# Performance work log

Measured on AMD Instinct MI355X. Metric: run time of the kernel, lower is better.

## Reference

```python
import jax, jax.numpy as jnp
import numpy as np

EPS = 1e-8  # F.cosine_similarity eps


def _cosine(nb, q):
    # nb: [N1, k, d], q: [N1, d] -> [N1, k]
    dot = jnp.einsum('nkd,nd->nk', nb, q)
    nb_norm = jnp.maximum(jnp.linalg.norm(nb, axis=-1), EPS)
    q_norm = jnp.maximum(jnp.linalg.norm(q, axis=-1), EPS)[:, None]
    return dot / (nb_norm * q_norm)


def setup_inputs() -> dict:
    key = jax.random.key(0)
    k0, k1, k2, k3 = jax.random.split(key, 4)
    N1, N2, D = 2048, 50000, 512
    return {
        'query_emb0': jax.random.normal(k0, (N1, D), dtype=jnp.float32),
        'query_emb1': jax.random.normal(k1, (N1, D), dtype=jnp.float32),
        'cand_emb0': jax.random.normal(k2, (N2, D), dtype=jnp.float32),
        'cand_emb1': jax.random.normal(k3, (N2, D), dtype=jnp.float32),
        'k': 32,
    }


def reference(query_emb0, query_emb1, cand_emb0, cand_emb1, k):
    # --- get_KNN_batch: L2 cdist on the ORIGINAL embeddings only (matches torch) ---
    # ||q - c||^2 = ||q||^2 + ||c||^2 - 2 q.c  (GEMM-based, compute-bound)
    q2 = jnp.sum(query_emb0 * query_emb0, axis=1, keepdims=True)       # [N1,1]
    c2 = jnp.sum(cand_emb0 * cand_emb0, axis=1)[None, :]               # [1,N2]
    d2 = jnp.maximum(q2 + c2 - 2.0 * (query_emb0 @ cand_emb0.T), 0.0)  # [N1,N2]
    dist = jnp.sqrt(d2)
    # topk of -distance == k nearest
    _, top_k_idx = jax.lax.top_k(-dist, k)                             # [N1,k]

    # --- get_neighbor_embeddings: gather both tables ---
    nb0 = cand_emb0[top_k_idx]  # [N1,k,d]
    nb1 = cand_emb1[top_k_idx]  # [N1,k,d]

    # --- compute_cosine_batch: elementwise max of the two cosine tables ---
    cos0 = _cosine(nb0, query_emb0)
    cos1 = _cosine(nb1, query_emb1)
    cosine_table = jnp.where(cos0 > cos1, cos0, cos1)                  # [N1,k]
    return cosine_table, jnp.mean(cosine_table, axis=-1)
```

## Files before the change

### kernel.cpp

```cpp
#include <hip/hip_runtime.h>
#include <math.h>


#define D       512
#define KSEL    32
#define NSELMX  64
#define NCF     8
#define TOPL    5
#define CEPS    1e-8f
#define INF     __builtin_inff()

#define MTF     64
#define NTF     256
#define KCF     32
#define NTHF    512

#define MT      64
#define NT      512
#define KC      64
#define NTH     512

using s16x8  = __attribute__((ext_vector_type(8)))  short;
using f32x16 = __attribute__((ext_vector_type(16))) float;

__device__ __forceinline__ void async16(const void* g, void* s) {
  __builtin_amdgcn_global_load_lds(
      (const __attribute__((address_space(1))) unsigned int*)g,
      (__attribute__((address_space(3))) unsigned int*)s, 16, 0, 0);
}

#define BARL() do { asm volatile("s_waitcnt lgkmcnt(0)" ::: "memory"); \
                    __builtin_amdgcn_s_barrier();                      \
                    asm volatile("" ::: "memory"); } while (0)

__device__ __forceinline__ unsigned int bfhi2(float x0, float x1) {
  unsigned int u0 = __float_as_uint(x0), u1 = __float_as_uint(x1);
  u0 = (u0 + 0x7fffu + ((u0 >> 16) & 1u)) >> 16;
  u1 = (u1 + 0x7fffu + ((u1 >> 16) & 1u)) & 0xffff0000u;
  return u0 | u1;
}

__global__ __launch_bounds__(256) void sumsq_cvt_kernel(
    const float* __restrict__ C, const float* __restrict__ Q,
    float* __restrict__ c2, float* __restrict__ q2,
    unsigned short* __restrict__ Cb, unsigned short* __restrict__ Qb,
    int n2, int n1)
{
  int wid  = threadIdx.x >> 6;
  int lane = threadIdx.x & 63;
  int row  = blockIdx.x * 4 + wid;
  const float* src; float* dst; unsigned short* bdst;
  if (row < n2) { src = C + (size_t)row * D; dst = c2 + row; bdst = Cb + (size_t)row * D; }
  else {
    int r = row - n2; if (r >= n1) return;
    src = Q + (size_t)r * D; dst = q2 + r; bdst = Qb + (size_t)r * D;
  }
  const float4* s4 = (const float4*)src;
  float4 a = s4[2*lane], b = s4[2*lane + 1];
  float s = a.x*a.x + a.y*a.y + a.z*a.z + a.w*a.w
          + b.x*b.x + b.y*b.y + b.z*b.z + b.w*b.w;
  int4 h;
  h.x = (int)bfhi2(a.x, a.y); h.y = (int)bfhi2(a.z, a.w);
  h.z = (int)bfhi2(b.x, b.y); h.w = (int)bfhi2(b.z, b.w);
  *(int4*)(bdst + 8*lane) = h;
  #pragma unroll
  for (int o = 32; o > 0; o >>= 1) s += __shfl_down(s, o, 64);
  if (lane == 0) *dst = s;
}

__global__ __launch_bounds__(256) void rows_sumsq_kernel(
    const float* __restrict__ C, const float* __restrict__ Q,
    float* __restrict__ c2, float* __restrict__ q2, int n2, int n1)
{
  int wid  = threadIdx.x >> 6;
  int lane = threadIdx.x & 63;
  int row  = blockIdx.x * 4 + wid;
  const float* src; float* dst;
  if (row < n2) { src = C + (size_t)row * D; dst = c2 + row; }
  else { int r = row - n2; if (r >= n1) return; src = Q + (size_t)r * D; dst = q2 + r; }
  const float4* s4 = (const float4*)src;
  float4 a = s4[lane], b = s4[lane + 64];
  float s = a.x*a.x + a.y*a.y + a.z*a.z + a.w*a.w
          + b.x*b.x + b.y*b.y + b.z*b.z + b.w*b.w;
  #pragma unroll
  for (int o = 32; o > 0; o >>= 1) s += __shfl_down(s, o, 64);
  if (lane == 0) *dst = s;
}

__device__ inline void worst_reduce(float dIn, int iIn, float& wd, int& wi) {
  float dd = dIn; int ii = iIn;
  #pragma unroll
  for (int o = 1; o <= 16; o <<= 1) {
    float dp = __shfl_xor(dd, o, 64);
    int   ip = __shfl_xor(ii, o, 64);
    bool take = (dp > dd) || (dp == dd && ip > ii);
    dd = take ? dp : dd; ii = take ? ip : ii;
  }
  wd = __shfl(dd, 0, 64); wi = __shfl(ii, 0, 64);
}

__device__ inline void cvt8(const float4 a, const float4 b, int4& hi, int4& lo) {
  float x[8] = {a.x, a.y, a.z, a.w, b.x, b.y, b.z, b.w};
  unsigned int hw[8], lw[8];
  #pragma unroll
  for (int j = 0; j < 8; ++j) {
    unsigned int ux = __float_as_uint(x[j]);
    unsigned int rh = (ux + 0x7fffu + ((ux >> 16) & 1u)) & 0xffff0000u;
    float rl = x[j] - __uint_as_float(rh);
    unsigned int ul = __float_as_uint(rl);
    hw[j] = rh >> 16;
    lw[j] = (ul + 0x7fffu + ((ul >> 16) & 1u)) >> 16;
  }
  hi = make_int4((int)(hw[0]|(hw[1]<<16)), (int)(hw[2]|(hw[3]<<16)),
                 (int)(hw[4]|(hw[5]<<16)), (int)(hw[6]|(hw[7]<<16)));
  lo = make_int4((int)(lw[0]|(lw[1]<<16)), (int)(lw[2]|(lw[3]<<16)),
                 (int)(lw[4]|(lw[5]<<16)), (int)(lw[6]|(lw[7]<<16)));
}

__global__ __launch_bounds__(NTHF, 2) void knn_phase1_bf_kernel(
    const unsigned short* __restrict__ Qb, const unsigned short* __restrict__ Cb,
    const float* __restrict__ q2g, const float* __restrict__ c2g,
    float* __restrict__ tkd, int* __restrict__ tki,
    int n1, int n2, int chunk, int nc)
{
  extern __shared__ char smem[];
  unsigned short* qs = (unsigned short*)smem;
  char* ringb = smem + 65536;
  float* dl   = (float*)(smem + 131072);

  const int tid  = threadIdx.x;
  const int w    = tid >> 6;
  const int l    = tid & 63;
  const int l31  = l & 31;
  const int half = l >> 5;
  const int bid     = blockIdx.x;
  const int chunkid = bid & (NCF - 1);
  const int mbase   = (bid >> 3) * MTF;
  const int cbase0  = chunkid * chunk;
  const int cend    = min(cbase0 + chunk, n2);

  float q2w[8];
  #pragma unroll
  for (int g = 0; g < 8; ++g)
    q2w[g] = q2g[min(mbase + (g>>2)*32 + w*4 + (g&3), n1 - 1)];

  unsigned long long vv[8][TOPL];
  #pragma unroll
  for (int g = 0; g < 8; ++g)
    #pragma unroll
    for (int t = 0; t < TOPL; ++t) vv[g][t] = 0xffffffffffffffffULL;

  float4 c2cur = *(const float4*)(c2g + cbase0 + 4*l);
  float4 c2nxt = c2cur;

  #pragma unroll
  for (int g = 0; g < 8; ++g) {
    int rho = w*8 + g;
    int gq  = min(mbase + rho, n1 - 1);
    const unsigned short* src = Qb + (size_t)gq * D + (size_t)((l ^ (rho & 7)) * 8);
    unsigned short* dst = qs + rho * 512;
    async16(src, dst);
  }

  auto STAGE = [&](int slot, int s4) {
    int t4 = s4 >> 4, kb4 = s4 & 15;
    #pragma unroll
    for (int i = 0; i < 2; ++i) {
      int cl  = w*32 + i*16 + (l >> 2);
      int gr  = cbase0 + t4*NTF + cl;
      int usr = (l & 3) ^ ((cl >> 1) & 3);
      const unsigned short* src = Cb + (size_t)gr * D + kb4*KCF + usr*8;
      unsigned short* dst = (unsigned short*)(ringb + slot*16384) + (w*32 + i*16)*32;
      async16(src, dst);
    }
  };

  f32x16 zf;
  #pragma unroll
  for (int e = 0; e < 16; ++e) zf[e] = 0.f;

  const int nst   = (cend - cbase0 + NTF - 1) / NTF;
  const int total = nst * 16;
  STAGE(0,0); STAGE(1,1); STAGE(2,2); STAGE(3,3);
  asm volatile("s_waitcnt vmcnt(6)" ::: "memory");
  __builtin_amdgcn_s_barrier();

  f32x16 acc[2];
  acc[0] = zf; acc[1] = zf;

  for (int nt = 0; nt < nst; ++nt) {
    const int cbase = cbase0 + nt * NTF;

    #pragma unroll
    for (int kb = 0; kb < 16; ++kb) {
      const int s   = nt*16 + kb;
      const int rem = total - 1 - s;
      if (rem > 2)       asm volatile("s_waitcnt vmcnt(6)" ::: "memory");
      else if (rem == 2) asm volatile("s_waitcnt vmcnt(4)" ::: "memory");
      else if (rem == 1) asm volatile("s_waitcnt vmcnt(2)" ::: "memory");
      else               asm volatile("s_waitcnt vmcnt(0)" ::: "memory");

      if (kb == 0 && nt + 1 < nst)
        c2nxt = *(const float4*)(c2g + cbase + NTF + 4*l);

      const unsigned short* cb_ =
          (const unsigned short*)(ringb + (s & 3)*16384) + (w*32 + l31)*32;
      #pragma unroll
      for (int ks = 0; ks < 2; ++ks) {
        int uc = (ks*2 + half) ^ ((l31 >> 1) & 3);
        s16x8 cf = *(const s16x8*)(cb_ + uc*8);
        #pragma unroll
        for (int qg = 0; qg < 2; ++qg) {
          int uq = (kb*4 + ks*2 + half) ^ (l31 & 7);
          s16x8 qf = *(const s16x8*)(qs + (qg*32 + l31)*512 + uq*8);
          acc[qg] = __builtin_amdgcn_mfma_f32_32x32x16_bf16(qf, cf, acc[qg], 0, 0, 0);
        }
      }
      if (s + 4 < total) {
        asm volatile("s_waitcnt lgkmcnt(0)" ::: "memory");
        STAGE(s & 3, s + 4);
      }
    }

    #pragma unroll
    for (int p = 0; p < 2; ++p) {
      #pragma unroll
      for (int r = 0; r < 16; ++r) {
        int rr = (r & 3) + 8*(r >> 2) + 4*half;
        dl[rr*NTF + w*32 + l31] = acc[p][r];
      }
      BARL();
      {
        float c2s[4] = {c2cur.x, c2cur.y, c2cur.z, c2cur.w};
        #pragma unroll
        for (int j = 0; j < 4; ++j) {
          const int g = p*4 + j;
          const float q2u = q2w[g];
          float4 sv4 = *((const float4*)(dl + (w*4 + j)*NTF) + l);
          float svs[4] = {sv4.x, sv4.y, sv4.z, sv4.w};
          #pragma unroll
          for (int jj = 0; jj < 4; ++jj) {
            int ci = cbase + 4*l + jj;
            if (ci < cend) {
              float d2v = fmaxf(q2u + c2s[jj] - 2.f*svs[jj], 0.f);
              unsigned long long e =
                  ((unsigned long long)__float_as_uint(d2v) << 32) | (unsigned int)ci;
              if (e < vv[g][TOPL-1]) {
                vv[g][TOPL-1] = e;
                #pragma unroll
                for (int t = TOPL-1; t > 0; --t) {
                  unsigned long long lo = vv[g][t-1] < vv[g][t] ? vv[g][t-1] : vv[g][t];
                  unsigned long long hi = vv[g][t-1] < vv[g][t] ? vv[g][t]   : vv[g][t-1];
                  vv[g][t-1] = lo; vv[g][t] = hi;
                }
              }
            }
          }
        }
      }
      BARL();
      acc[p] = zf;
    }
    c2cur = c2nxt;
  }

  unsigned long long* sel = (unsigned long long*)smem + (size_t)w * 512;
  const unsigned long long mlt = (l == 0) ? 0ull : ((~0ull) >> (64 - l));
  __syncthreads();
  #pragma unroll
  for (int g = 0; g < 8; ++g) {
    unsigned int pk = (unsigned int)(vv[g][0] >> 32);
    #pragma unroll
    for (int o = 1; o < 64; o <<= 1) {
      unsigned int other = (unsigned int)__shfl_xor((int)pk, o, 64);
      pk = (other > pk) ? other : pk;
    }
    int cnt = 0;
    #pragma unroll
    for (int t = 0; t < TOPL; ++t) cnt += ((unsigned int)(vv[g][t] >> 32) <= pk) ? 1 : 0;
    unsigned long long b0 = __ballot(cnt & 1);
    unsigned long long b1 = __ballot(cnt & 2);
    unsigned long long b2 = __ballot(cnt & 4);
    int pre = __popcll(b0 & mlt) + 2*__popcll(b1 & mlt) + 4*__popcll(b2 & mlt);
    int Ns  = __popcll(b0) + 2*__popcll(b1) + 4*__popcll(b2);
    #pragma unroll
    for (int t = 0; t < TOPL; ++t)
      if (t < cnt) sel[pre + t] = vv[g][t];
    asm volatile("s_waitcnt lgkmcnt(0)" ::: "memory");
    __builtin_amdgcn_sched_barrier(0);
    int rk[TOPL];
    #pragma unroll
    for (int t = 0; t < TOPL; ++t) rk[t] = 0;
    for (int j = 0; j < Ns; ++j) {
      unsigned long long e = sel[j];
      #pragma unroll
      for (int t = 0; t < TOPL; ++t) rk[t] += (e < vv[g][t]) ? 1 : 0;
    }
    int gq = mbase + (g>>2)*32 + w*4 + (g&3);
    if (gq < n1) {
      #pragma unroll
      for (int t = 0; t < TOPL; ++t)
        if (t < cnt && rk[t] < KSEL) {
          size_t o = ((size_t)gq * nc + chunkid) * KSEL + rk[t];
          tkd[o] = __uint_as_float((unsigned int)(vv[g][t] >> 32));
          tki[o] = (int)(unsigned int)(vv[g][t] & 0xffffffffu);
        }
    }
  }
}

__global__ __launch_bounds__(NTH) void knn_phase1_cvt_kernel(
    const float* __restrict__ Q, const float* __restrict__ C,
    const float* __restrict__ q2g, const float* __restrict__ c2g,
    float* __restrict__ tkd, int* __restrict__ tki,
    int n1, int n2, int chunk, int nc)
{
  extern __shared__ char smem[];
  unsigned short* qh = (unsigned short*)smem;
  unsigned short* ql = qh + 64*64;
  unsigned short* ch = ql + 64*64;
  unsigned short* cl = ch + 512*64;
  float* dl = (float*)(smem + 147456);

  const int tid  = threadIdx.x;
  const int w    = tid >> 6;
  const int l    = tid & 63;
  const int l31  = l & 31;
  const int half = l >> 5;
  const int mbase   = blockIdx.x * MT;
  const int chunkid = blockIdx.y;
  const int cbase0  = chunkid * chunk;
  const int cend    = min(cbase0 + chunk, n2);

  float q2w[8];
  #pragma unroll
  for (int g = 0; g < 8; ++g) q2w[g] = q2g[min(mbase + g*8 + w, n1 - 1)];

  float listd[8]; int listi[8]; float wd4[8]; int wi4[8];
  #pragma unroll
  for (int g = 0; g < 8; ++g) { listd[g]=INF; listi[g]=0x7fffffff; wd4[g]=INF; wi4[g]=0x7fffffff; }

  const int srow = tid >> 3;
  const int sk8  = (tid & 7) * 8;
  const int su   = (tid & 7);

  float4 cva[8][2], qva[2];
  auto LOADR = [&](int kb, int cb) {
    {
      int gr = min(mbase + srow, n1 - 1);
      const float4* p = (const float4*)(Q + (size_t)gr * D + kb*KC + sk8);
      qva[0] = p[0]; qva[1] = p[1];
    }
    #pragma unroll
    for (int r = 0; r < 8; ++r) {
      int gn = cb + srow + 64*r;
      if (gn < cend) {
        const float4* p = (const float4*)(C + (size_t)gn * D + kb*KC + sk8);
        cva[r][0] = p[0]; cva[r][1] = p[1];
      } else {
        cva[r][0] = make_float4(0.f,0.f,0.f,0.f);
        cva[r][1] = make_float4(0.f,0.f,0.f,0.f);
      }
    }
  };
  auto STORE = [&]() {
    int4 hi, lo;
    {
      int idx = srow*64 + (su ^ (srow & 7))*8;
      cvt8(qva[0], qva[1], hi, lo);
      *(int4*)(qh + idx) = hi; *(int4*)(ql + idx) = lo;
    }
    #pragma unroll
    for (int r = 0; r < 8; ++r) {
      int row = srow + 64*r;
      int idx = row*64 + (su ^ (row & 7))*8;
      cvt8(cva[r][0], cva[r][1], hi, lo);
      *(int4*)(ch + idx) = hi; *(int4*)(cl + idx) = lo;
    }
  };

  f32x16 zf;
  #pragma unroll
  for (int e = 0; e < 16; ++e) zf[e] = 0.f;

  const int nsteps = (cend - cbase0 + NT - 1) / NT;
  LOADR(0, cbase0);

  for (int nt = 0; nt < nsteps; ++nt) {
    const int cbase = cbase0 + nt * NT;
    f32x16 acc[2][2];
    #pragma unroll
    for (int rt = 0; rt < 2; ++rt)
      #pragma unroll
      for (int ct = 0; ct < 2; ++ct) acc[rt][ct] = zf;

    for (int kb = 0; kb < D/KC; ++kb) {
      __syncthreads();
      STORE();
      __syncthreads();
      if (kb + 1 < D/KC)        LOADR(kb + 1, cbase);
      else if (nt + 1 < nsteps) LOADR(0, cbase + NT);

      #pragma unroll
      for (int ks = 0; ks < 4; ++ks) {
        const int u = 2*ks + half;
        s16x8 qf[2][2], cf[2][2];
        #pragma unroll
        for (int rt = 0; rt < 2; ++rt) {
          int r = rt*32 + l31;
          int idx = r*64 + (u ^ (r & 7))*8;
          qf[rt][0] = *(const s16x8*)(qh + idx);
          qf[rt][1] = *(const s16x8*)(ql + idx);
        }
        #pragma unroll
        for (int ct = 0; ct < 2; ++ct) {
          int c = w*64 + ct*32 + l31;
          int idx = c*64 + (u ^ (c & 7))*8;
          cf[ct][0] = *(const s16x8*)(ch + idx);
          cf[ct][1] = *(const s16x8*)(cl + idx);
        }
        #pragma unroll
        for (int rt = 0; rt < 2; ++rt)
          #pragma unroll
          for (int ct = 0; ct < 2; ++ct) {
            acc[rt][ct] = __builtin_amdgcn_mfma_f32_32x32x16_bf16(qf[rt][0], cf[ct][0], acc[rt][ct], 0, 0, 0);
            acc[rt][ct] = __builtin_amdgcn_mfma_f32_32x32x16_bf16(qf[rt][0], cf[ct][1], acc[rt][ct], 0, 0, 0);
            acc[rt][ct] = __builtin_amdgcn_mfma_f32_32x32x16_bf16(qf[rt][1], cf[ct][0], acc[rt][ct], 0, 0, 0);
          }
      }
    }

    float c2v[2]; int vld[2];
    #pragma unroll
    for (int ct = 0; ct < 2; ++ct) {
      int gc = cbase + w*64 + ct*32 + l31;
      vld[ct] = (gc < cend);
      c2v[ct] = vld[ct] ? c2g[gc] : 0.f;
    }
    #pragma unroll
    for (int g = 0; g < 8; ++g) {
      const int rt = g >> 2, qq = g & 3;
      #pragma unroll
      for (int jj = 0; jj < 4; ++jj)
        #pragma unroll
        for (int ct = 0; ct < 2; ++ct) {
          float a = acc[rt][ct][4*qq + jj];
          float s = c2v[ct] - 2.f * a;
          dl[(4*half + jj)*512 + w*64 + ct*32 + l31] = vld[ct] ? s : INF;
        }
      __syncthreads();
      const float q2u = q2w[g];
      #pragma unroll
      for (int j2 = 0; j2 < 8; ++j2) {
        float sv = dl[w*512 + l + 64*j2];
        float dv = sqrtf(fmaxf(q2u + sv, 0.f));
        unsigned long long mask = __ballot(dv < wd4[g]);
        while (mask) {
          int L = __ffsll(mask) - 1; mask &= mask - 1;
          float dnew = __shfl(dv, L, 64);
          int ci = cbase + 64*j2 + L;
          if ((dnew < wd4[g]) || (dnew == wd4[g] && ci < wi4[g])) {
            bool isw = (l < 32) && (listd[g] == wd4[g]) && (listi[g] == wi4[g]);
            int wl = __ffsll(__ballot(isw)) - 1;
            if (l == wl) { listd[g] = dnew; listi[g] = ci; }
            worst_reduce((l < 32) ? listd[g] : -1.f,
                         (l < 32) ? listi[g] : -1, wd4[g], wi4[g]);
          }
        }
      }
      __syncthreads();
    }
  }

  #pragma unroll
  for (int g = 0; g < 8; ++g) {
    int gq = mbase + g*8 + w;
    float d = listd[g]; int i = listi[g];
    int rank = 0;
    #pragma unroll
    for (int j = 0; j < KSEL; ++j) {
      float dj = __shfl(listd[g], j, 64);
      int   ij = __shfl(listi[g], j, 64);
      rank += (dj < d) || (dj == d && ij < i);
    }
    if (l < 32 && gq < n1) {
      size_t o = ((size_t)gq * nc + chunkid) * KSEL + rank;
      tkd[o] = d; tki[o] = i;
    }
  }
}

__global__ __launch_bounds__(256) void knn_phase2_kernel(
    const float* __restrict__ Q0, const float* __restrict__ Q1,
    const float* __restrict__ C0, const float* __restrict__ C1,
    const float* __restrict__ q2g, const float* __restrict__ c2g,
    const float* __restrict__ tkd, const int* __restrict__ tki,
    float* __restrict__ out, int n1, int n2, int nc)
{
  __shared__ float q0s[D], q1s[D];
  __shared__ float pd[256]; __shared__ int pi[256];
  __shared__ float nd[NSELMX]; __shared__ int ni[NSELMX];
  __shared__ float de[NSELMX];
  __shared__ int   fi[KSEL];
  __shared__ float cosj[KSEL];
  __shared__ float red0[4], red1[4], qn[2];

  const int q = blockIdx.x, tid = threadIdx.x;
  const int npool = nc * KSEL;
  const int nsel  = (NSELMX < npool) ? NSELMX : npool;

  if (tid < 128) ((float4*)q0s)[tid] = ((const float4*)(Q0 + (size_t)q*D))[tid];
  else           ((float4*)q1s)[tid-128] = ((const float4*)(Q1 + (size_t)q*D))[tid-128];
  if (tid < npool) { pd[tid] = tkd[(size_t)q*npool + tid]; pi[tid] = tki[(size_t)q*npool + tid]; }
  __syncthreads();

  float a0 = q0s[tid], b0 = q0s[tid+256], a1 = q1s[tid], b1 = q1s[tid+256];
  float s0 = a0*a0 + b0*b0, s1 = a1*a1 + b1*b1;
  #pragma unroll
  for (int o = 32; o > 0; o >>= 1) { s0 += __shfl_down(s0, o, 64); s1 += __shfl_down(s1, o, 64); }
  int lane = tid & 63, wid = tid >> 6;
  if (lane == 0) { red0[wid] = s0; red1[wid] = s1; }

  if (tid < npool) {
    float dm = pd[tid]; int im = pi[tid]; int rank = 0;
    for (int j = 0; j < npool; ++j) {
      float dj = pd[j]; int ij = pi[j];
      rank += (dj < dm) || (dj == dm && ij < im);
    }
    if (rank < nsel) { nd[rank] = dm; ni[rank] = im; }
  }
  __syncthreads();
  if (tid == 0) {
    qn[0] = fmaxf(sqrtf(red0[0]+red0[1]+red0[2]+red0[3]), CEPS);
    qn[1] = fmaxf(sqrtf(red1[0]+red1[1]+red1[2]+red1[3]), CEPS);
  }

  const float q2q = q2g[q];
  const int ll = tid & 7;
  for (int base = 0; base < NSELMX; base += 32) {
    int g = base + (tid >> 3);
    if (g < nsel) {
      int ix = ni[g];
      bool okx = (ix >= 0 && ix < n2);
      int ixc = okx ? ix : 0;
      const float4* r0  = (const float4*)(C0 + (size_t)ixc * D);
      const float4* q04 = (const float4*)q0s;
      float dot = 0.f;
      #pragma unroll
      for (int r = 0; r < 16; ++r) {
        float4 v = r0[r*8 + ll], u = q04[r*8 + ll];
        dot = fmaf(v.x,u.x, fmaf(v.y,u.y, fmaf(v.z,u.z, fmaf(v.w,u.w, dot))));
      }
      #pragma unroll
      for (int o = 4; o > 0; o >>= 1) dot += __shfl_xor(dot, o, 64);
      if (ll == 0) de[g] = okx ? sqrtf(fmaxf(q2q + c2g[ixc] - 2.f*dot, 0.f)) : INF;
    }
  }
  __syncthreads();

  if (tid < nsel) {
    float dm = de[tid]; int im = ni[tid]; int rank = 0;
    for (int j = 0; j < nsel; ++j) {
      float dj = de[j]; int ij = ni[j];
      rank += (dj < dm) || (dj == dm && ij < im);
    }
    if (rank < KSEL) fi[rank] = im;
  }
  __syncthreads();

  const int g = tid >> 3;
  int ix = fi[g];
  ix = (ix >= 0 && ix < n2) ? ix : 0;
  const float4* r0  = (const float4*)(C0 + (size_t)ix * D);
  const float4* r1  = (const float4*)(C1 + (size_t)ix * D);
  const float4* q04 = (const float4*)q0s;
  const float4* q14 = (const float4*)q1s;
  float dot0 = 0.f, nn0 = 0.f, dot1 = 0.f, nn1 = 0.f;
  #pragma unroll
  for (int r = 0; r < 16; ++r) {
    int e4 = r*8 + ll;
    float4 v0 = r0[e4], qv0 = q04[e4];
    dot0 = fmaf(v0.x,qv0.x, fmaf(v0.y,qv0.y, fmaf(v0.z,qv0.z, fmaf(v0.w,qv0.w, dot0))));
    nn0  = fmaf(v0.x,v0.x,  fmaf(v0.y,v0.y,  fmaf(v0.z,v0.z,  fmaf(v0.w,v0.w,  nn0))));
    float4 v1 = r1[e4], qv1 = q14[e4];
    dot1 = fmaf(v1.x,qv1.x, fmaf(v1.y,qv1.y, fmaf(v1.z,qv1.z, fmaf(v1.w,qv1.w, dot1))));
    nn1  = fmaf(v1.x,v1.x,  fmaf(v1.y,v1.y,  fmaf(v1.z,v1.z,  fmaf(v1.w,v1.w,  nn1))));
  }
  #pragma unroll
  for (int o = 4; o > 0; o >>= 1) {
    dot0 += __shfl_xor(dot0, o, 64); nn0 += __shfl_xor(nn0, o, 64);
    dot1 += __shfl_xor(dot1, o, 64); nn1 += __shfl_xor(nn1, o, 64);
  }
  if (ll == 0) {
    float c0 = dot0 / (fmaxf(sqrtf(nn0), CEPS) * qn[0]);
    float c1 = dot1 / (fmaxf(sqrtf(nn1), CEPS) * qn[1]);
    float cv = (c0 > c1) ? c0 : c1;
    out[(size_t)q * KSEL + g] = cv;
    cosj[g] = cv;
  }
  __syncthreads();
  if (tid == 0) {
    float s = 0.f;
    #pragma unroll
    for (int j = 0; j < KSEL; ++j) s += cosj[j];
    out[(size_t)n1 * KSEL + q] = s * (1.f / KSEL);
  }
}

extern "C" void kernel_launch(void* const* d_in, const int* in_sizes, int n_in,
                              void* d_out, int out_size, void* d_ws, size_t ws_size,
                              hipStream_t stream)
{
  const float* Q0 = (const float*)d_in[0];
  const float* Q1 = (const float*)d_in[1];
  const float* C0 = (const float*)d_in[2];
  const float* C1 = (const float*)d_in[3];
  const int n1 = in_sizes[0] / D;
  const int n2 = in_sizes[2] / D;
  float* out = (float*)d_out;
  if (n1 <= 0 || n2 <= 0) return;

  char* wsb = (char*)d_ws;
  size_t c2n = ((size_t)n2 + 127) & ~(size_t)127;
  size_t q2n = ((size_t)n1 + 127) & ~(size_t)127;

  size_t off_c2  = 0;
  size_t off_q2  = off_c2 + c2n*4;
  size_t off_tkd = off_q2 + q2n*4;
  size_t off_tki = off_tkd + (size_t)n1*NCF*KSEL*4;
  size_t off_cb  = (off_tki + (size_t)n1*NCF*KSEL*4 + 255) & ~(size_t)255;
  size_t off_qb  = off_cb + ((size_t)n2 + 512)*D*2;
  size_t need    = off_qb + (size_t)n1*D*2;
  bool fast = (ws_size >= need);

  if (fast) {
    float* c2  = (float*)(wsb + off_c2);
    float* q2  = (float*)(wsb + off_q2);
    float* tkd = (float*)(wsb + off_tkd);
    int*   tki = (int*)(wsb + off_tki);
    unsigned short* Cb = (unsigned short*)(wsb + off_cb);
    unsigned short* Qb = (unsigned short*)(wsb + off_qb);

    sumsq_cvt_kernel<<<(n2 + n1 + 3)/4, 256, 0, stream>>>(C0, Q0, c2, q2, Cb, Qb, n2, n1);

    const int chunk  = (n2 + NCF - 1) / NCF;
    const int mtiles = (n1 + MTF - 1) / MTF;
    (void)hipFuncSetAttribute((const void*)knn_phase1_bf_kernel,
                              hipFuncAttributeMaxDynamicSharedMemorySize, 163840);
    knn_phase1_bf_kernel<<<mtiles * NCF, NTHF, 163840, stream>>>(
        Qb, Cb, q2, c2, tkd, tki, n1, n2, chunk, NCF);
    knn_phase2_kernel<<<n1, 256, 0, stream>>>(Q0, Q1, C0, C1, q2, c2, tkd, tki, out, n1, n2, NCF);
  } else {
    float* wsf = (float*)d_ws;
    int nc = 8;
    while (nc > 1 && (c2n + q2n + (size_t)n1 * nc * KSEL * 2) * 4 > ws_size) nc >>= 1;
    float* c2  = wsf;
    float* q2  = wsf + c2n;
    float* tkd = wsf + c2n + q2n;
    int*   tki = (int*)(wsf + c2n + q2n + (size_t)n1 * nc * KSEL);

    rows_sumsq_kernel<<<(n2 + n1 + 3)/4, 256, 0, stream>>>(C0, Q0, c2, q2, n2, n1);
    const int chunk  = (n2 + nc - 1) / nc;
    const int mtiles = (n1 + MT - 1) / MT;
    (void)hipFuncSetAttribute((const void*)knn_phase1_cvt_kernel,
                              hipFuncAttributeMaxDynamicSharedMemorySize, 163840);
    knn_phase1_cvt_kernel<<<dim3(mtiles, nc), NTH, 163840, stream>>>(
        Q0, C0, q2, c2, tkd, tki, n1, n2, chunk, nc);
    knn_phase2_kernel<<<n1, 256, 0, stream>>>(Q0, Q1, C0, C1, q2, c2, tkd, tki, out, n1, n2, nc);
  }
}
```

Measured before the change: 472.9 us.

## Load candidate fragments directly from global into registers, dropping LDS ring

Replaces the async global-to-LDS staging ring for candidate tiles with direct per-lane global loads into a four-deep register prefetch buffer. Each wave now reads its own candidate rows straight into MFMA operands, which removes the LDS round-trip, the lgkmcnt waits and the manual vmcnt bookkeeping. The c2 prefetch is simplified to a load at the start of each tile. Dynamic shared memory drops from 160KB to 96KB, which may allow more resident blocks. In exchange, global loads are less coalesced and latency hiding depends on the compiler scheduling the register prefetch.

```diff
diff --git a/kernel.cpp b/kernel.cpp
--- a/kernel.cpp
+++ b/kernel.cpp
@@ -12,7 +12,6 @@
 
 #define MTF     64
 #define NTF     256
-#define KCF     32
 #define NTHF    512
 
 #define MT      64
@@ -125,8 +124,7 @@
 {
   extern __shared__ char smem[];
   unsigned short* qs = (unsigned short*)smem;
-  char* ringb = smem + 65536;
-  float* dl   = (float*)(smem + 131072);
+  float* dl = (float*)(smem + 65536);
 
   const int tid  = threadIdx.x;
   const int w    = tid >> 6;
@@ -150,9 +148,6 @@
     #pragma unroll
     for (int t = 0; t < TOPL; ++t) vv[g][t] = 0xffffffffffffffffULL;
 
-  float4 c2cur = *(const float4*)(c2g + cbase0 + 4*l);
-  float4 c2nxt = c2cur;
-
   #pragma unroll
   for (int g = 0; g < 8; ++g) {
     int rho = w*8 + g;
@@ -161,19 +156,8 @@
     unsigned short* dst = qs + rho * 512;
     async16(src, dst);
   }
-
-  auto STAGE = [&](int slot, int s4) {
-    int t4 = s4 >> 4, kb4 = s4 & 15;
-    #pragma unroll
-    for (int i = 0; i < 2; ++i) {
-      int cl  = w*32 + i*16 + (l >> 2);
-      int gr  = cbase0 + t4*NTF + cl;
-      int usr = (l & 3) ^ ((cl >> 1) & 3);
-      const unsigned short* src = Cb + (size_t)gr * D + kb4*KCF + usr*8;
-      unsigned short* dst = (unsigned short*)(ringb + slot*16384) + (w*32 + i*16)*32;
-      async16(src, dst);
-    }
-  };
+  asm volatile("s_waitcnt vmcnt(0)" ::: "memory");
+  __builtin_amdgcn_s_barrier();
 
   f32x16 zf;
   #pragma unroll
@@ -181,44 +165,55 @@
 
   const int nst   = (cend - cbase0 + NTF - 1) / NTF;
   const int total = nst * 16;
-  STAGE(0,0); STAGE(1,1); STAGE(2,2); STAGE(3,3);
-  asm volatile("s_waitcnt vmcnt(6)" ::: "memory");
-  __builtin_amdgcn_s_barrier();
+
+  const unsigned short* cptr =
+      Cb + (size_t)(cbase0 + w*32 + l31) * D + half*8;
+  s16x8 pa0a, pa0b, pa1a, pa1b, pa2a, pa2b, pa3a, pa3b;
+  pa0a = *(const s16x8*)cptr; pa0b = *(const s16x8*)(cptr + 16); cptr += 32;
+  pa1a = *(const s16x8*)cptr; pa1b = *(const s16x8*)(cptr + 16); cptr += 32;
+  pa2a = *(const s16x8*)cptr; pa2b = *(const s16x8*)(cptr + 16); cptr += 32;
+  pa3a = *(const s16x8*)cptr; pa3b = *(const s16x8*)(cptr + 16); cptr += 32;
 
   f32x16 acc[2];
   acc[0] = zf; acc[1] = zf;
 
   for (int nt = 0; nt < nst; ++nt) {
     const int cbase = cbase0 + nt * NTF;
+    float4 c2cur;
 
     #pragma unroll
     for (int kb = 0; kb < 16; ++kb) {
-      const int s   = nt*16 + kb;
-      const int rem = total - 1 - s;
-      if (rem > 2)       asm volatile("s_waitcnt vmcnt(6)" ::: "memory");
-      else if (rem == 2) asm volatile("s_waitcnt vmcnt(4)" ::: "memory");
-      else if (rem == 1) asm volatile("s_waitcnt vmcnt(2)" ::: "memory");
-      else               asm volatile("s_waitcnt vmcnt(0)" ::: "memory");
-
-      if (kb == 0 && nt + 1 < nst)
-        c2nxt = *(const float4*)(c2g + cbase + NTF + 4*l);
-
-      const unsigned short* cb_ =
-          (const unsigned short*)(ringb + (s & 3)*16384) + (w*32 + l31)*32;
-      #pragma unroll
-      for (int ks = 0; ks < 2; ++ks) {
-        int uc = (ks*2 + half) ^ ((l31 >> 1) & 3);
-        s16x8 cf = *(const s16x8*)(cb_ + uc*8);
-        #pragma unroll
-        for (int qg = 0; qg < 2; ++qg) {
-          int uq = (kb*4 + ks*2 + half) ^ (l31 & 7);
-          s16x8 qf = *(const s16x8*)(qs + (qg*32 + l31)*512 + uq*8);
-          acc[qg] = __builtin_amdgcn_mfma_f32_32x32x16_bf16(qf, cf, acc[qg], 0, 0, 0);
+      const int s = nt*16 + kb;
+      if (kb == 0) c2cur = *(const float4*)(c2g + cbase + 4*l);
+
+      s16x8 cf0, cf1;
+      switch (kb & 3) {
+        case 0: cf0 = pa0a; cf1 = pa0b; break;
+        case 1: cf0 = pa1a; cf1 = pa1b; break;
+        case 2: cf0 = pa2a; cf1 = pa2b; break;
+        default: cf0 = pa3a; cf1 = pa3b; break;
+      }
+      #pragma unroll
+      for (int qg = 0; qg < 2; ++qg) {
+        int uq0 = (kb*4 + 0*2 + half) ^ (l31 & 7);
+        int uq1 = (kb*4 + 1*2 + half) ^ (l31 & 7);
+        s16x8 qf0 = *(const s16x8*)(qs + (qg*32 + l31)*512 + uq0*8);
+        s16x8 qf1 = *(const s16x8*)(qs + (qg*32 + l31)*512 + uq1*8);
+        acc[qg] = __builtin_amdgcn_mfma_f32_32x32x16_bf16(qf0, cf0, acc[qg], 0, 0, 0);
+        acc[qg] = __builtin_amdgcn_mfma_f32_32x32x16_bf16(qf1, cf1, acc[qg], 0, 0, 0);
+      }
+      if (s + 4 < total) {
+        s16x8 na = *(const s16x8*)cptr;
+        s16x8 nb = *(const s16x8*)(cptr + 16);
+        switch (kb & 3) {
+          case 0: pa0a = na; pa0b = nb; break;
+          case 1: pa1a = na; pa1b = nb; break;
+          case 2: pa2a = na; pa2b = nb; break;
+          default: pa3a = na; pa3b = nb; break;
         }
-      }
-      if (s + 4 < total) {
-        asm volatile("s_waitcnt lgkmcnt(0)" ::: "memory");
-        STAGE(s & 3, s + 4);
+        cptr += 32;
+        if (((kb + 5) & 15) == 0)
+          cptr += (size_t)NTF * D - 512;
       }
     }
 
@@ -261,7 +256,6 @@
       BARL();
       acc[p] = zf;
     }
-    c2cur = c2nxt;
   }
 
   unsigned long long* sel = (unsigned long long*)smem + (size_t)w * 512;
@@ -646,8 +640,8 @@
     const int chunk  = (n2 + NCF - 1) / NCF;
     const int mtiles = (n1 + MTF - 1) / MTF;
     (void)hipFuncSetAttribute((const void*)knn_phase1_bf_kernel,
-                              hipFuncAttributeMaxDynamicSharedMemorySize, 163840);
-    knn_phase1_bf_kernel<<<mtiles * NCF, NTHF, 163840, stream>>>(
+                              hipFuncAttributeMaxDynamicSharedMemorySize, 98304);
+    knn_phase1_bf_kernel<<<mtiles * NCF, NTHF, 98304, stream>>>(
         Qb, Cb, q2, c2, tkd, tki, n1, n2, chunk, NCF);
     knn_phase2_kernel<<<n1, 256, 0, stream>>>(Q0, Q1, C0, C1, q2, c2, tkd, tki, out, n1, n2, NCF);
   } else {
```

After: 538.8 us. 13.9% more time.
